# Optimization experiments

Measured on AMD Instinct MI355X. Metric: run time of the kernel, lower is better.

The kernel has to match this reference:

```python
import jax, jax.numpy as jnp
import numpy as np

B, T, C = 4, 1024, 1024
HEAD_SIZE = 64
H = C // HEAD_SIZE
N_LAYER, LAYER_ID = 24, 12
D_MIX_LORA, D_DECAY_LORA = 32, 64
HEAD_SIZE_DIVISOR = 8
LN_EPS = 1e-5 * HEAD_SIZE_DIVISOR ** 2


def setup_inputs() -> dict:
    key = jax.random.key(0)
    ks = jax.random.split(key, 16)
    x = jax.random.normal(ks[0], (B, T, C), jnp.float32)

    r01 = LAYER_ID / (N_LAYER - 1)          # ratio_0_to_1
    r10 = 1.0 - LAYER_ID / N_LAYER          # ratio_1_to_almost0
    ddd = np.arange(C, dtype=np.float64) / C

    time_maa_x = jnp.asarray((1.0 - ddd ** r10).astype(np.float32))
    time_maa_w = jnp.asarray((1.0 - ddd ** r10).astype(np.float32))
    time_maa_k = jnp.asarray((1.0 - ddd ** r10).astype(np.float32))
    time_maa_v = jnp.asarray((1.0 - (ddd ** r10 + 0.3 * r01)).astype(np.float32))
    time_maa_r = jnp.asarray((1.0 - ddd ** (0.5 * r10)).astype(np.float32))
    time_maa_g = jnp.asarray((1.0 - ddd ** (0.5 * r10)).astype(np.float32))

    n = np.arange(C, dtype=np.float64)
    time_decay = jnp.asarray((-6.0 + 5.0 * (n / (C - 1)) ** (0.7 + 1.3 * r01)).astype(np.float32))
    zigzag = ((n + 1) % 3 - 1) * 0.1
    time_faaaa = jnp.asarray((r01 * (1.0 - n / (C - 1)) + zigzag).astype(np.float32)).reshape(H, HEAD_SIZE)

    u = lambda k, shp: jax.random.uniform(k, shp, jnp.float32, -0.01, 0.01)
    time_maa_w1 = u(ks[1], (C, D_MIX_LORA * 5))   # zeros in orig init; small random for a non-trivial test
    time_maa_w2 = u(ks[2], (5, D_MIX_LORA, C))
    time_decay_w1 = u(ks[3], (C, D_DECAY_LORA))
    time_decay_w2 = u(ks[4], (D_DECAY_LORA, C))

    s = 1.0 / np.sqrt(C)
    Wr = jax.random.normal(ks[5], (C, C), jnp.float32) * s   # stored [in, out]
    Wk = jax.random.normal(ks[6], (C, C), jnp.float32) * s
    Wv = jax.random.normal(ks[7], (C, C), jnp.float32) * s
    Wg = jax.random.normal(ks[8], (C, C), jnp.float32) * s
    Wo = jax.random.normal(ks[9], (C, C), jnp.float32) * s
    ln_w = jnp.ones((C,), jnp.float32)
    ln_b = jnp.zeros((C,), jnp.float32)

    return dict(x=x, time_maa_x=time_maa_x, time_maa_w=time_maa_w, time_maa_k=time_maa_k,
                time_maa_v=time_maa_v, time_maa_r=time_maa_r, time_maa_g=time_maa_g,
                time_maa_w1=time_maa_w1, time_maa_w2=time_maa_w2,
                time_decay=time_decay, time_decay_w1=time_decay_w1, time_decay_w2=time_decay_w2,
                time_faaaa=time_faaaa, Wr=Wr, Wk=Wk, Wv=Wv, Wg=Wg, Wo=Wo, ln_w=ln_w, ln_b=ln_b)


def _wkv6(r, k, v, w, u):
    # r,k,v,w: [B,T,H,N]; u: [H,N]. Data-dependent linear recurrence per head.
    def step(S, inp):               # S: [B,H,N,N] (key dim j, value dim i)
        r_t, k_t, v_t, w_t = inp    # each [B,H,N]
        y = jnp.einsum('bhj,bhji->bhi', r_t, S) \
            + jnp.sum(r_t * u * k_t, axis=-1, keepdims=True) * v_t
        decay = jnp.exp(-jnp.exp(w_t))            # CUDA kernel: w_eff = exp(-exp(w))
        S = decay[..., None] * S + k_t[..., None] * v_t[..., None, :]
        return S, y

    to_t = lambda a: jnp.transpose(a, (1, 0, 2, 3))  # [T,B,H,N]
    S0 = jnp.zeros(r.shape[:1] + (r.shape[2], r.shape[3], r.shape[3]), r.dtype)
    _, ys = jax.lax.scan(step, S0, (to_t(r), to_t(k), to_t(v), to_t(w)))
    return jnp.transpose(ys, (1, 0, 2, 3))            # [B,T,H,N]


def reference(x, time_maa_x, time_maa_w, time_maa_k, time_maa_v, time_maa_r, time_maa_g,
              time_maa_w1, time_maa_w2, time_decay, time_decay_w1, time_decay_w2,
              time_faaaa, Wr, Wk, Wv, Wg, Wo, ln_w, ln_b):
    b, t, c = x.shape
    h, n = H, HEAD_SIZE

    # token shift: ZeroPad2d((0,0,1,-1)) shifts time right by one with zero pad
    xx = jnp.concatenate([jnp.zeros_like(x[:, :1]), x[:, :-1]], axis=1) - x
    xxx = x + xx * time_maa_x
    mix = jnp.tanh(xxx @ time_maa_w1).reshape(b, t, 5, D_MIX_LORA)
    m = jnp.einsum('btsd,sdc->sbtc', mix, time_maa_w2)  # [5,B,T,C]
    xw = x + xx * (time_maa_w + m[0])
    xk = x + xx * (time_maa_k + m[1])
    xv = x + xx * (time_maa_v + m[2])
    xr = x + xx * (time_maa_r + m[3])
    xg = x + xx * (time_maa_g + m[4])

    r = xr @ Wr
    k = xk @ Wk
    v = xv @ Wv
    g = jax.nn.silu(xg @ Wg)
    w = time_decay + jnp.tanh(xw @ time_decay_w1) @ time_decay_w2

    y = _wkv6(r.reshape(b, t, h, n), k.reshape(b, t, h, n),
              v.reshape(b, t, h, n), w.reshape(b, t, h, n), time_faaaa)

    # GroupNorm with n_head groups over channel dim, eps = 1e-5 * divisor^2
    mu = y.mean(-1, keepdims=True)
    var = y.var(-1, keepdims=True)
    yn = ((y - mu) / jnp.sqrt(var + LN_EPS)).reshape(b, t, c) * ln_w + ln_b

    return (yn * g) @ Wo
```

## Files before the change

### kernel.cpp

```cpp
#include <hip/hip_runtime.h>

typedef unsigned short u16;
typedef short short8 __attribute__((ext_vector_type(8)));
typedef short short4v __attribute__((ext_vector_type(4)));
typedef float float4v __attribute__((ext_vector_type(4)));
typedef unsigned uint4v __attribute__((ext_vector_type(4)));

__device__ __forceinline__ float bf2f(u16 h) { return __uint_as_float(((unsigned)h) << 16); }
__device__ __forceinline__ u16 f2bf(float f) {
  unsigned u = __float_as_uint(f);
  unsigned r = (u + 0x7fffu + ((u >> 16) & 1u)) >> 16;
  return (u16)r;
}
__device__ __forceinline__ bool is_f32(const void* probe) {
  return ((const u16*)probe)[0] != 0x3F80;
}
__device__ __forceinline__ float ldin(const void* p, long i, bool f32m) {
  return f32m ? ((const float*)p)[i] : bf2f(((const u16*)p)[i]);
}

typedef __attribute__((address_space(1))) const unsigned int as1_u32;
typedef __attribute__((address_space(3))) unsigned int as3_u32;
__device__ __forceinline__ void gl2lds16(const void* g, void* l) {
  __builtin_amdgcn_global_load_lds((as1_u32*)g, (as3_u32*)l, 16, 0, 0);
}

template <int CTRL>
__device__ __forceinline__ float dpp_add(float x) {
  int s = __builtin_amdgcn_update_dpp(0, __float_as_int(x), CTRL, 0xF, 0xF, true);
  return x + __int_as_float(s);
}

__global__ __launch_bounds__(256) void sentinel_fill(u16* o, long n) {
  long i = (long)blockIdx.x * 256 + threadIdx.x;
  if (i < n) o[i] = 0x42C8;
}

struct TDescArr {
  const void* src[13];
  u16* dst[13];
  int rows[13];
  int cols[13];
  int roff[13];
};

__global__ __launch_bounds__(256) void transpose_all(TDescArr d, const void* probe) {
  bool f32m = is_f32(probe);
  int z = blockIdx.z;
  int rows = d.rows[z], cols = d.cols[z], roff = d.roff[z];
  int bc = blockIdx.x * 32, br = blockIdx.y * 32;
  if (bc >= cols || br >= rows) return;
  const void* src = d.src[z];
  u16* dst = d.dst[z];
  __shared__ u16 tile[32][33];
  int tx = threadIdx.x & 31, ty = threadIdx.x >> 5;
#pragma unroll
  for (int i = 0; i < 32; i += 8)
    tile[ty + i][tx] = f2bf(ldin(src, (long)(roff + br + ty + i) * cols + bc + tx, f32m));
  __syncthreads();
#pragma unroll
  for (int i = 0; i < 32; i += 8)
    dst[(long)(bc + ty + i) * rows + br + tx] = tile[tx][ty + i];
}

__global__ __launch_bounds__(256) void token_shift(const void* __restrict__ x,
                                                   const void* __restrict__ maa_x,
                                                   u16* __restrict__ xxx) {
  bool f32m = is_f32(maa_x);
  long idx = (long)blockIdx.x * 256 + threadIdx.x;
  int c = (int)(idx & 1023);
  int tt = (int)((idx >> 10) & 1023);
  float xv = ldin(x, idx, f32m);
  float xp = tt > 0 ? ldin(x, idx - 1024, f32m) : 0.f;
  xxx[idx] = f2bf(xv + (xp - xv) * ldin(maa_x, c, f32m));
}

template <int EPI>
__device__ __forceinline__ void gemm128_core(const u16* __restrict__ A,
                                             const u16* __restrict__ Bt,
                                             void* __restrict__ Cv, int N, int K,
                                             int m0, int n0, u16* As, u16* Bs,
                                             bool f32m) {
  int t = threadIdx.x, lane = t & 63, w = t >> 6;
  int wm = (w >> 1) * 64, wn = (w & 1) * 64;
  int lr = lane & 15, lk = lane >> 4;
  float4v acc[4][4];
#pragma unroll
  for (int i = 0; i < 4; i++)
#pragma unroll
    for (int j = 0; j < 4; j++) acc[i][j] = (float4v){0.f, 0.f, 0.f, 0.f};
  int srow = t >> 3;
  int scol = ((t & 7) ^ (srow & 7)) * 8;
  const u16* Ag = A + (long)(m0 + srow) * K + scol;
  const u16* Bg = Bt + (long)(n0 + srow) * K + scol;
  int so = w * 512;
  for (int k0 = 0; k0 < K; k0 += 64) {
    __syncthreads();
#pragma unroll
    for (int p = 0; p < 4; p++) {
      gl2lds16(Ag + (long)p * 32 * K + k0, As + p * 2048 + so);
      gl2lds16(Bg + (long)p * 32 * K + k0, Bs + p * 2048 + so);
    }
    __syncthreads();
    short8 af[4][2], bfr[4][2];
#pragma unroll
    for (int i = 0; i < 4; i++) {
      int R = wm + i * 16 + lr;
#pragma unroll
      for (int h = 0; h < 2; h++) {
        int j = h * 4 + lk;
        af[i][h] = *(const short8*)(As + R * 64 + (j ^ (R & 7)) * 8);
      }
    }
#pragma unroll
    for (int i = 0; i < 4; i++) {
      int R = wn + i * 16 + lr;
#pragma unroll
      for (int h = 0; h < 2; h++) {
        int j = h * 4 + lk;
        bfr[i][h] = *(const short8*)(Bs + R * 64 + (j ^ (R & 7)) * 8);
      }
    }
#pragma unroll
    for (int mi2 = 0; mi2 < 4; mi2++)
#pragma unroll
      for (int ni2 = 0; ni2 < 4; ni2++) {
        acc[mi2][ni2] = __builtin_amdgcn_mfma_f32_16x16x32_bf16(
            af[mi2][0], bfr[ni2][0], acc[mi2][ni2], 0, 0, 0);
        acc[mi2][ni2] = __builtin_amdgcn_mfma_f32_16x16x32_bf16(
            af[mi2][1], bfr[ni2][1], acc[mi2][ni2], 0, 0, 0);
      }
  }
#pragma unroll
  for (int mi2 = 0; mi2 < 4; mi2++) {
#pragma unroll
    for (int ni2 = 0; ni2 < 4; ni2++) {
      int col = n0 + wn + ni2 * 16 + lr;
#pragma unroll
      for (int rr = 0; rr < 4; rr++) {
        long row = m0 + wm + mi2 * 16 + lk * 4 + rr;
        float val = acc[mi2][ni2][rr];
        if (EPI == 1) val = val / (1.f + __expf(-val));
        if (EPI == 2 && f32m) ((float*)Cv)[row * N + col] = val;
        else ((u16*)Cv)[row * N + col] = f2bf(val);
      }
    }
  }
}

template <int EPI>
__global__ __launch_bounds__(256, 2) void gemm_big(const u16* __restrict__ A,
                                                   const u16* __restrict__ Bt,
                                                   void* __restrict__ Cv, int M, int N,
                                                   int K, const void* probe) {
  __shared__ alignas(16) u16 As[128 * 64];
  __shared__ alignas(16) u16 Bs[128 * 64];
  int sid = blockIdx.y * gridDim.x + blockIdx.x;
  int per8 = (gridDim.x * gridDim.y) >> 3;
  int L = (sid & 7) * per8 + (sid >> 3);
  int mi = L / gridDim.y, ni = L % gridDim.y;
  bool f32m = (EPI == 2) ? is_f32(probe) : false;
  gemm128_core<EPI>(A, Bt, Cv, N, K, mi * 128, ni * 128, As, Bs, f32m);
}

template <int EPI0, int EPI1>
__global__ __launch_bounds__(256, 2) void gemm_big2(
    const u16* __restrict__ A0, const u16* __restrict__ Bt0, u16* __restrict__ C0,
    const u16* __restrict__ A1, const u16* __restrict__ Bt1, u16* __restrict__ C1,
    int M, int N, int K) {
  __shared__ alignas(16) u16 As[128 * 64];
  __shared__ alignas(16) u16 Bs[128 * 64];
  int z = blockIdx.z;
  int sid = blockIdx.y * gridDim.x + blockIdx.x;
  int per8 = (gridDim.x * gridDim.y) >> 3;
  int L = (sid & 7) * per8 + (sid >> 3);
  int mi = L / gridDim.y, ni = L % gridDim.y;
  if (z == 0)
    gemm128_core<EPI0>(A0, Bt0, C0, N, K, mi * 128, ni * 128, As, Bs, false);
  else
    gemm128_core<EPI1>(A1, Bt1, C1, N, K, mi * 128, ni * 128, As, Bs, false);
}

template <int EPI>
__global__ __launch_bounds__(256) void gemm_wave(const u16* __restrict__ A, int lda,
                                                 const u16* __restrict__ Bt,
                                                 u16* __restrict__ C, int ldc,
                                                 float* dA_, float* dB_, int Ntot,
                                                 int K, const void* aux0,
                                                 const void* probe,
                                                 const void* __restrict__ xin) {
  int t = threadIdx.x, lane = t & 63, w = t >> 6;
  int m0 = blockIdx.x * 64 + w * 16;
  int span = Ntot / gridDim.y;
  int col0 = blockIdx.y * span;
  const u16* Bp = Bt + (long)col0 * K;
  int lr = lane & 15, lk = lane >> 4;
  bool f32m = (EPI >= 2) ? is_f32(probe) : false;
  int nt = span >> 4;
  for (int g0 = 0; g0 < nt; g0 += 4) {
    int gc = (nt - g0 < 4) ? (nt - g0) : 4;
    float4v acc[4];
#pragma unroll
    for (int i = 0; i < 4; i++) acc[i] = (float4v){0.f, 0.f, 0.f, 0.f};
    for (int k0 = 0; k0 < K; k0 += 32) {
      short8 a = *(const short8*)(A + (long)(m0 + lr) * lda + k0 + lk * 8);
      for (int gi = 0; gi < gc; gi++) {
        int n0 = (g0 + gi) * 16;
        short8 b = *(const short8*)(Bp + (long)(n0 + lr) * K + k0 + lk * 8);
        acc[gi] = __builtin_amdgcn_mfma_f32_16x16x32_bf16(a, b, acc[gi], 0, 0, 0);
      }
    }
    for (int gi = 0; gi < gc; gi++) {
      int col = col0 + (g0 + gi) * 16 + lr;
      if (EPI == 3) {
        long r0 = m0 + lk * 4;
        float xv4[4];
#pragma unroll
        for (int rr = 0; rr < 4; rr++)
          xv4[rr] = ldin(xin, (r0 + rr) * 1024 + col, f32m);
        float xpv = ((int)(r0 & 1023) > 0) ? ldin(xin, (r0 - 1) * 1024 + col, f32m) : 0.f;
        float mv = ldin(aux0, col, f32m);
#pragma unroll
        for (int rr = 0; rr < 4; rr++) {
          float xv = xv4[rr];
          float xp = (rr == 0) ? xpv : xv4[rr - 1];
          C[(r0 + rr) * 1024 + col] = f2bf(xv + (xp - xv) * (mv + acc[gi][rr]));
        }
      } else {
#pragma unroll
        for (int rr = 0; rr < 4; rr++) {
          long row = m0 + lk * 4 + rr;
          float val = acc[gi][rr];
          if (EPI == 0) {
            C[row * ldc + col] = f2bf(val);
          } else if (EPI == 1) {
            float vv = fminf(fmaxf(val, -15.f), 15.f);
            float e = __expf(2.f * vv);
            C[row * ldc + col] = f2bf((e - 1.f) / (e + 1.f));
          } else if (EPI == 2) {
            float wv = val + ldin(aux0, col, f32m);
            float ew = __expf(wv);
            if (row < 2048) dA_[row * 1024 + col] = ew;
            else dB_[(row - 2048) * 1024 + col] = ew;
          }
        }
      }
    }
  }
}

__global__ __launch_bounds__(256) void gemm_wave3_pair(
    const u16* __restrict__ A0, const u16* __restrict__ Bt0, u16* __restrict__ C0,
    const void* __restrict__ maa0, const u16* __restrict__ A1,
    const u16* __restrict__ Bt1, u16* __restrict__ C1,
    const void* __restrict__ maa1, const void* probe,
    const void* __restrict__ xin) {
  int z = blockIdx.z;
  const u16* A = z ? A1 : A0;
  const u16* Bt = z ? Bt1 : Bt0;
  u16* C = z ? C1 : C0;
  const void* maa = z ? maa1 : maa0;
  bool f32m = is_f32(probe);
  int t = threadIdx.x, lane = t & 63, w = t >> 6;
  int m0 = blockIdx.x * 64 + w * 16;
  int col0 = blockIdx.y * 32;
  const u16* Bp = Bt + (long)col0 * 32;
  int lr = lane & 15, lk = lane >> 4;
  float4v acc[2];
  acc[0] = (float4v){0.f, 0.f, 0.f, 0.f};
  acc[1] = (float4v){0.f, 0.f, 0.f, 0.f};
  short8 a = *(const short8*)(A + (long)(m0 + lr) * 160 + lk * 8);
#pragma unroll
  for (int gi = 0; gi < 2; gi++) {
    short8 b = *(const short8*)(Bp + (long)(gi * 16 + lr) * 32 + lk * 8);
    acc[gi] = __builtin_amdgcn_mfma_f32_16x16x32_bf16(a, b, acc[gi], 0, 0, 0);
  }
#pragma unroll
  for (int gi = 0; gi < 2; gi++) {
    int col = col0 + gi * 16 + lr;
    long r0 = m0 + lk * 4;
    float xv4[4];
#pragma unroll
    for (int rr = 0; rr < 4; rr++)
      xv4[rr] = ldin(xin, (r0 + rr) * 1024 + col, f32m);
    float xpv = ((int)(r0 & 1023) > 0) ? ldin(xin, (r0 - 1) * 1024 + col, f32m) : 0.f;
    float mv = ldin(maa, col, f32m);
#pragma unroll
    for (int rr = 0; rr < 4; rr++) {
      float xv = xv4[rr];
      float xp = (rr == 0) ? xpv : xv4[rr - 1];
      C[(r0 + rr) * 1024 + col] = f2bf(xv + (xp - xv) * (mv + acc[gi][rr]));
    }
  }
}

__global__ __launch_bounds__(256) void gemm_n64_tanh(const u16* __restrict__ A,
                                                     const u16* __restrict__ Bt,
                                                     u16* __restrict__ C) {
  int t = threadIdx.x, lane = t & 63, w = t >> 6;
  int m0 = blockIdx.x * 16;
  int n0 = w * 16;
  int lr = lane & 15, lk = lane >> 4;
  float4v acc = (float4v){0.f, 0.f, 0.f, 0.f};
  const u16* Ap = A + (long)(m0 + lr) * 1024;
  const u16* Bp = Bt + (long)(n0 + lr) * 1024;
  for (int k0 = 0; k0 < 1024; k0 += 32) {
    short8 a = *(const short8*)(Ap + k0 + lk * 8);
    short8 b = *(const short8*)(Bp + k0 + lk * 8);
    acc = __builtin_amdgcn_mfma_f32_16x16x32_bf16(a, b, acc, 0, 0, 0);
  }
#pragma unroll
  for (int rr = 0; rr < 4; rr++) {
    long row = m0 + lk * 4 + rr;
    float vv = fminf(fmaxf(acc[rr], -15.f), 15.f);
    float e = __expf(2.f * vv);
    C[row * 64 + n0 + lr] = f2bf((e - 1.f) / (e + 1.f));
  }
}

__global__ __launch_bounds__(512) void wkv6_chunk(
    const u16* __restrict__ r, const u16* __restrict__ k, const u16* __restrict__ v,
    const float* __restrict__ ewA, const float* __restrict__ ewB,
    const void* __restrict__ u_, const void* probe, u16* __restrict__ y) {
  bool f32m = is_f32(probe);
  int bh = blockIdx.x;
  int b = bh >> 4, h = bh & 15;
  int tid = threadIdx.x, lane = tid & 63, w = tid >> 6;
  int lr = lane & 15, lk = lane >> 4;

  __shared__ alignas(16) float raw[32][68];
  __shared__ alignas(16) float scc[2][32][68];
  __shared__ alignas(16) u16 Rp[32][72];
  __shared__ alignas(16) u16 Kp[32][72];
  __shared__ alignas(16) u16 KdF[64 * 40 + 56];
  __shared__ alignas(16) u16 Vt[64][40];
  __shared__ alignas(16) u16 Pb[32][40];
  __shared__ alignas(16) u16 Sh[64][72];
  __shared__ alignas(16) u16 Sl[64][72];
  __shared__ float diag32[32];

  const long base = ((long)b << 20) + h * 64;
  const float* ewg =
      (b < 2 ? ewA + (long)b * 1048576 : ewB + (long)(b - 2) * 1048576) + h * 64;

  int tt = tid >> 4, kg4 = tid & 15;
  int ck = (w & 3) * 16 + (lane & 15);
  int cq = lane >> 4;
  float u4[4];
#pragma unroll
  for (int i = 0; i < 4; i++) u4[i] = ldin(u_, h * 64 + kg4 * 4 + i, f32m);

  int kw = (w & 3) * 16, vq = w >> 2;
  int skey = kw + lk * 4;
  int yt = w >> 2, yv = w & 3;

  float4v Sst[2];
  Sst[0] = (float4v){0.f, 0.f, 0.f, 0.f};
  Sst[1] = (float4v){0.f, 0.f, 0.f, 0.f};

  {
    long grow = (long)tt << 10;
    float4v ewq = *(const float4v*)(ewg + grow + kg4 * 4);
    short4v rraw = *(const short4v*)(r + base + grow + kg4 * 4);
    short4v kraw = *(const short4v*)(k + base + grow + kg4 * 4);
    short4v vraw = *(const short4v*)(v + base + grow + kg4 * 4);
    *(float4v*)&raw[tt][kg4 * 4] = ewq;
    __syncthreads();
    if (w < 4) {
      float pseg[8];
      float s = 0.f;
#pragma unroll
      for (int j = 0; j < 8; j++) {
        s += raw[cq * 8 + j][ck];
        pseg[j] = s;
      }
      float tot = pseg[7], x = tot;
      float up = __shfl_up(x, 16);
      if (cq >= 1) x += up;
      up = __shfl_up(x, 32);
      if (cq >= 2) x += up;
      float pre = x - tot;
#pragma unroll
      for (int j = 0; j < 8; j++) scc[0][cq * 8 + j][ck] = pre + pseg[j];
    }
    __syncthreads();
    {
      float pd = 0.f;
      short4v rpv, kpv;
#pragma unroll
      for (int i = 0; i < 4; i++) {
        int key = kg4 * 4 + i;
        float rf = bf2f((u16)rraw[i]);
        float kf = bf2f((u16)kraw[i]);
        float si = scc[0][tt][key];
        float sx = tt ? scc[0][tt - 1][key] : 0.f;
        float sE = scc[0][31][key];
        rpv[i] = (short)f2bf(rf * __expf(-sx));
        kpv[i] = (short)f2bf(kf * __expf(si));
        KdF[key * 40 + ((key >> 3) & 7) * 8 + tt] = f2bf(kf * __expf(si - sE));
        pd = fmaf(rf * u4[i], kf, pd);
      }
      *(short4v*)&Rp[tt][kg4 * 4] = rpv;
      *(short4v*)&Kp[tt][kg4 * 4] = kpv;
      pd = dpp_add<0xB1>(pd);
      pd = dpp_add<0x4E>(pd);
      pd = dpp_add<0x104>(pd);
      pd = dpp_add<0x108>(pd);
      if (kg4 == 0) diag32[tt] = pd;
    }
#pragma unroll
    for (int i = 0; i < 4; i++) Vt[kg4 * 4 + i][tt] = (u16)vraw[i];
#pragma unroll
    for (int vt = 0; vt < 2; vt++) {
      short4v z4 = (short4v){0, 0, 0, 0};
      *(short4v*)&Sh[vq * 32 + vt * 16 + lr][skey] = z4;
      *(short4v*)&Sl[vq * 32 + vt * 16 + lr][skey] = z4;
    }
    __syncthreads();
  }

  for (int ci = 0; ci < 32; ++ci) {
    int c0 = ci << 5;
    int c0n = (ci == 31) ? c0 : c0 + 32;
    int pc = ci & 1, pn = pc ^ 1;
    long grow = (long)(c0n + tt) << 10;
    float4v ewq = *(const float4v*)(ewg + grow + kg4 * 4);
    short4v rraw = *(const short4v*)(r + base + grow + kg4 * 4);
    short4v kraw = *(const short4v*)(k + base + grow + kg4 * 4);
    short4v vraw = *(const short4v*)(v + base + grow + kg4 * 4);

    if (w < 4) {
      int pt = w >> 1, pj = w & 1;
      float4v pacc = (float4v){0.f, 0.f, 0.f, 0.f};
      short8 aP0 = *(const short8*)&Rp[pt * 16 + lr][lk * 8];
      short8 aP1 = *(const short8*)&Rp[pt * 16 + lr][lk * 8 + 32];
      short8 bP0 = *(const short8*)&Kp[pj * 16 + lr][lk * 8];
      short8 bP1 = *(const short8*)&Kp[pj * 16 + lr][lk * 8 + 32];
      pacc = __builtin_amdgcn_mfma_f32_16x16x32_bf16(aP0, bP0, pacc, 0, 0, 0);
      pacc = __builtin_amdgcn_mfma_f32_16x16x32_bf16(aP1, bP1, pacc, 0, 0, 0);
      int jcol = pj * 16 + lr;
#pragma unroll
      for (int rr = 0; rr < 4; rr++) {
        int trow = pt * 16 + lk * 4 + rr;
        float val = (jcol < trow) ? pacc[rr] : (jcol == trow ? diag32[trow] : 0.f);
        Pb[trow][jcol] = f2bf(val);
      }
    }
    *(float4v*)&raw[tt][kg4 * 4] = ewq;
    __syncthreads();

    if (w < 4) {
      float pseg[8];
      float s = 0.f;
#pragma unroll
      for (int j = 0; j < 8; j++) {
        s += raw[cq * 8 + j][ck];
        pseg[j] = s;
      }
      float tot = pseg[7], x = tot;
      float up = __shfl_up(x, 16);
      if (cq >= 1) x += up;
      up = __shfl_up(x, 32);
      if (cq >= 2) x += up;
      float pre = x - tot;
#pragma unroll
      for (int j = 0; j < 8; j++) scc[pn][cq * 8 + j][ck] = pre + pseg[j];
    }
    {
      float4v yacc = (float4v){0.f, 0.f, 0.f, 0.f};
      short8 aY = *(const short8*)&Pb[yt * 16 + lr][lk * 8];
      short8 bY = *(const short8*)&Vt[yv * 16 + lr][lk * 8];
      yacc = __builtin_amdgcn_mfma_f32_16x16x32_bf16(aY, bY, yacc, 0, 0, 0);
      short8 aR0 = *(const short8*)&Rp[yt * 16 + lr][lk * 8];
      short8 aR1 = *(const short8*)&Rp[yt * 16 + lr][lk * 8 + 32];
      short8 bH0 = *(const short8*)&Sh[yv * 16 + lr][lk * 8];
      short8 bH1 = *(const short8*)&Sh[yv * 16 + lr][lk * 8 + 32];
      short8 bL0 = *(const short8*)&Sl[yv * 16 + lr][lk * 8];
      short8 bL1 = *(const short8*)&Sl[yv * 16 + lr][lk * 8 + 32];
      yacc = __builtin_amdgcn_mfma_f32_16x16x32_bf16(aR0, bH0, yacc, 0, 0, 0);
      yacc = __builtin_amdgcn_mfma_f32_16x16x32_bf16(aR1, bH1, yacc, 0, 0, 0);
      yacc = __builtin_amdgcn_mfma_f32_16x16x32_bf16(aR0, bL0, yacc, 0, 0, 0);
      yacc = __builtin_amdgcn_mfma_f32_16x16x32_bf16(aR1, bL1, yacc, 0, 0, 0);
#pragma unroll
      for (int rr = 0; rr < 4; rr++) {
        int trow = yt * 16 + lk * 4 + rr;
        y[base + ((long)(c0 + trow) << 10) + yv * 16 + lr] = f2bf(yacc[rr]);
      }
      int kr = kw + lr;
      short8 aS = *(const short8*)&KdF[kr * 40 + ((kr >> 3) & 7) * 8 + lk * 8];
      short8 bS0 = *(const short8*)&Vt[vq * 32 + lr][lk * 8];
      short8 bS1 = *(const short8*)&Vt[vq * 32 + 16 + lr][lk * 8];
      float4v sa0 = (float4v){0.f, 0.f, 0.f, 0.f};
      float4v sa1 = (float4v){0.f, 0.f, 0.f, 0.f};
      sa0 = __builtin_amdgcn_mfma_f32_16x16x32_bf16(aS, bS0, sa0, 0, 0, 0);
      sa1 = __builtin_amdgcn_mfma_f32_16x16x32_bf16(aS, bS1, sa1, 0, 0, 0);
#pragma unroll
      for (int rr = 0; rr < 4; rr++) {
        float cl = __expf(-scc[pc][31][skey + rr]);
        Sst[0][rr] = fmaf(Sst[0][rr], cl, sa0[rr]);
        Sst[1][rr] = fmaf(Sst[1][rr], cl, sa1[rr]);
      }
    }
    __syncthreads();

    {
      float pd = 0.f;
      short4v rpv, kpv;
#pragma unroll
      for (int i = 0; i < 4; i++) {
        int key = kg4 * 4 + i;
        float rf = bf2f((u16)rraw[i]);
        float kf = bf2f((u16)kraw[i]);
        float si = scc[pn][tt][key];
        float sx = tt ? scc[pn][tt - 1][key] : 0.f;
        float sE = scc[pn][31][key];
        rpv[i] = (short)f2bf(rf * __expf(-sx));
        kpv[i] = (short)f2bf(kf * __expf(si));
        KdF[key * 40 + ((key >> 3) & 7) * 8 + tt] = f2bf(kf * __expf(si - sE));
        pd = fmaf(rf * u4[i], kf, pd);
      }
      *(short4v*)&Rp[tt][kg4 * 4] = rpv;
      *(short4v*)&Kp[tt][kg4 * 4] = kpv;
      pd = dpp_add<0xB1>(pd);
      pd = dpp_add<0x4E>(pd);
      pd = dpp_add<0x104>(pd);
      pd = dpp_add<0x108>(pd);
      if (kg4 == 0) diag32[tt] = pd;
    }
#pragma unroll
    for (int i = 0; i < 4; i++) Vt[kg4 * 4 + i][tt] = (u16)vraw[i];
#pragma unroll
    for (int vt = 0; vt < 2; vt++) {
      short4v hi4, lo4;
#pragma unroll
      for (int rr = 0; rr < 4; rr++) {
        u16 hv = f2bf(Sst[vt][rr]);
        hi4[rr] = (short)hv;
        lo4[rr] = (short)f2bf(Sst[vt][rr] - bf2f(hv));
      }
      *(short4v*)&Sh[vq * 32 + vt * 16 + lr][skey] = hi4;
      *(short4v*)&Sl[vq * 32 + vt * 16 + lr][skey] = lo4;
    }
    __syncthreads();
  }
}

__global__ __launch_bounds__(256) void gn_gate(const u16* __restrict__ y,
                                               const u16* __restrict__ g,
                                               const void* __restrict__ lnw,
                                               const void* __restrict__ lnb,
                                               const void* probe,
                                               u16* __restrict__ out) {
  bool f32m = is_f32(probe);
  int gid = blockIdx.x * 4 + (threadIdx.x >> 6);
  int lane = threadIdx.x & 63;
  int h = gid & 15;
  long row = gid >> 4;
  long off = row * 1024 + h * 64 + lane;
  float val = bf2f(y[off]);
  float s = val, sq = val * val;
#pragma unroll
  for (int m = 1; m < 64; m <<= 1) {
    s += __shfl_xor(s, m);
    sq += __shfl_xor(sq, m);
  }
  float mean = s * (1.f / 64.f);
  float var = fmaxf(sq * (1.f / 64.f) - mean * mean, 0.f);
  float inv = rsqrtf(var + 6.4e-4f);
  int c = h * 64 + lane;
  float yn = (val - mean) * inv * ldin(lnw, c, f32m) + ldin(lnb, c, f32m);
  out[off] = f2bf(yn * bf2f(g[off]));
}

extern "C" void kernel_launch(void* const* d_in, const int* in_sizes, int n_in,
                              void* d_out, int out_size, void* d_ws, size_t ws_size,
                              hipStream_t stream) {
  const void* x = d_in[0];
  const void* maaX = d_in[1];
  const void* maa_s[5] = {d_in[2], d_in[3], d_in[4], d_in[5], d_in[6]};
  const void* w1 = d_in[7];
  const void* w2 = d_in[8];
  const void* tdec = d_in[9];
  const void* dw1 = d_in[10];
  const void* dw2 = d_in[11];
  const void* faaaa = d_in[12];
  const void* Wr = d_in[13];
  const void* Wk = d_in[14];
  const void* Wv = d_in[15];
  const void* Wg = d_in[16];
  const void* Wo = d_in[17];
  const void* lnw = d_in[18];
  const void* lnb = d_in[19];

  const long oWoT = 4194304;
  const long ow1T = 5242880;
  const long odw1T = 5406720;
  const long odw2T = 5472256;
  const long ow2T = 5537792;
  const long omixb = 5701632;
  const long owtan = 6356992;
  const long oxxxg = 6619136;
  const long omx = 10813440;
  const long orb = 15007744;
  const long okb = 19202048;
  const long ovb = 23396352;
  const long oyb = 27590656;
  const long oend = 31784960;
  const size_t needed = (size_t)oend * 2;

  if (ws_size < needed) {
    sentinel_fill<<<dim3((unsigned)((out_size + 255) / 256)), 256, 0, stream>>>(
        (u16*)d_out, out_size);
    return;
  }

  u16* W = (u16*)d_ws;
  u16* WrT = W;
  u16* WkT = W + 1048576;
  u16* WvT = W + 2097152;
  u16* WgT = W + 3145728;
  u16* WoT = W + oWoT;
  u16* w1T = W + ow1T;
  u16* dw1T = W + odw1T;
  u16* dw2T = W + odw2T;
  u16* w2T = W + ow2T;
  u16* mixb = W + omixb;
  u16* wtan = W + owtan;
  u16* xxxg = W + oxxxg;
  u16* mx = W + omx;
  u16* rbuf = W + orb;
  u16* kbuf = W + okb;
  u16* vbuf = W + ovb;
  u16* ybuf = W + oyb;
  float* dA_ = (float*)W;
  float* dB_ = (float*)(W + omx);
  u16* gated = mx;

  TDescArr td;
  const void* s5[5] = {Wr, Wk, Wv, Wg, Wo};
  u16* t5[5] = {WrT, WkT, WvT, WgT, WoT};
  for (int i = 0; i < 13; i++) td.roff[i] = 0;
  for (int i = 0; i < 5; i++) {
    td.src[i] = s5[i]; td.dst[i] = t5[i]; td.rows[i] = 1024; td.cols[i] = 1024;
  }
  td.src[5] = w1;  td.dst[5] = w1T;  td.rows[5] = 1024; td.cols[5] = 160;
  td.src[6] = dw1; td.dst[6] = dw1T; td.rows[6] = 1024; td.cols[6] = 64;
  td.src[7] = dw2; td.dst[7] = dw2T; td.rows[7] = 64;   td.cols[7] = 1024;
  for (int s = 0; s < 5; s++) {
    td.src[8 + s] = w2;
    td.dst[8 + s] = w2T + s * 1024 * 32;
    td.rows[8 + s] = 32; td.cols[8 + s] = 1024; td.roff[8 + s] = s * 32;
  }

  transpose_all<<<dim3(32, 32, 13), 256, 0, stream>>>(td, maaX);
  token_shift<<<dim3(16384), 256, 0, stream>>>(x, maaX, xxxg);
  gemm_wave<1><<<dim3(64, 10), 256, 0, stream>>>(xxxg, 1024, w1T, mixb, 160, nullptr,
                                                 nullptr, 160, 1024, nullptr, nullptr,
                                                 nullptr);
  gemm_wave3_pair<<<dim3(64, 32, 2), 256, 0, stream>>>(
      mixb + 3 * 32, w2T + 3 * 32768, mx, maa_s[3],
      mixb + 1 * 32, w2T + 1 * 32768, ybuf, maa_s[1], maaX, x);
  gemm_big2<0, 0><<<dim3(32, 8, 2), 256, 0, stream>>>(mx, WrT, rbuf, ybuf, WkT, kbuf,
                                                      4096, 1024, 1024);
  gemm_wave3_pair<<<dim3(64, 32, 2), 256, 0, stream>>>(
      mixb + 2 * 32, w2T + 2 * 32768, mx, maa_s[2],
      mixb + 4 * 32, w2T + 4 * 32768, ybuf, maa_s[4], maaX, x);
  gemm_big2<0, 1><<<dim3(32, 8, 2), 256, 0, stream>>>(mx, WvT, vbuf, ybuf, WgT, xxxg,
                                                      4096, 1024, 1024);
  gemm_wave<3><<<dim3(64, 32), 256, 0, stream>>>(mixb + 0 * 32, 160, w2T + 0 * 32768,
                                                 mx, 1024, nullptr, nullptr, 1024, 32,
                                                 maa_s[0], maaX, x);
  gemm_n64_tanh<<<dim3(256), 256, 0, stream>>>(mx, dw1T, wtan);
  gemm_wave<2><<<dim3(64, 16), 256, 0, stream>>>(wtan, 64, dw2T, nullptr, 0, dA_, dB_,
                                                 1024, 64, tdec, maaX, nullptr);
  wkv6_chunk<<<dim3(64), 512, 0, stream>>>(rbuf, kbuf, vbuf, dA_, dB_, faaaa, maaX,
                                           ybuf);
  gn_gate<<<dim3(16384), 256, 0, stream>>>(ybuf, xxxg, lnw, lnb, maaX, gated);
  gemm_big<2><<<dim3(32, 8), 256, 0, stream>>>(gated, WoT, d_out, 4096, 1024, 1024, maaX);
}
```

Measured before the change: 353.5 us.

## Split WKV6 scan into parallel segment-state pass and per-segment output pass

The single-pass chunked WKV6 kernel, which ran one block per (batch, head) over 32 sequential chunks, is split in two. The first kernel computes per-segment state contributions and decay products for three of the four 256-token segments. The second kernel runs 256 blocks; each combines the preceding segment states and then processes its own 8 chunks. This adds parallelism, since the original kernel used only 64 blocks on a GPU with many more CUs. The cost is an extra launch, scratch traffic through the output buffer, redundant prefix combination, and splitting the state into bf16 hi/lo parts at each segment start.

```diff
diff --git a/kernel.cpp b/kernel.cpp
--- a/kernel.cpp
+++ b/kernel.cpp
@@ -318,12 +318,112 @@
   }
 }
 
-__global__ __launch_bounds__(512) void wkv6_chunk(
+__global__ __launch_bounds__(512) void wkv6_pass1(
+    const u16* __restrict__ k, const u16* __restrict__ v,
+    const float* __restrict__ ewA, const float* __restrict__ ewB,
+    float* __restrict__ Ascr, float* __restrict__ Dscr) {
+  int bx = blockIdx.x;
+  int g = bx >> 6, bh = bx & 63;
+  int b = bh >> 4, h = bh & 15;
+  int tid = threadIdx.x, lane = tid & 63, w = tid >> 6;
+  int lr = lane & 15, lk = lane >> 4;
+
+  __shared__ alignas(16) float raw[32][68];
+  __shared__ alignas(16) float sck[32][68];
+  __shared__ alignas(16) u16 KdF[64 * 40 + 56];
+  __shared__ alignas(16) u16 Vt[64][40];
+
+  const long base = ((long)b << 20) + h * 64;
+  const float* ewg =
+      (b < 2 ? ewA + (long)b * 1048576 : ewB + (long)(b - 2) * 1048576) + h * 64;
+
+  int tt = tid >> 4, kg4 = tid & 15;
+  int ck = (w & 3) * 16 + (lane & 15), cq = lane >> 4;
+  int kw = (w & 3) * 16, vq = w >> 2;
+  int skey = kw + lk * 4;
+
+  float4v Sst[2];
+  Sst[0] = (float4v){0.f, 0.f, 0.f, 0.f};
+  Sst[1] = (float4v){0.f, 0.f, 0.f, 0.f};
+  float Dacc[4] = {1.f, 1.f, 1.f, 1.f};
+
+  for (int cc = g * 8; cc < g * 8 + 8; ++cc) {
+    long grow = (long)(cc * 32 + tt) << 10;
+    float4v ewq = *(const float4v*)(ewg + grow + kg4 * 4);
+    short4v kraw = *(const short4v*)(k + base + grow + kg4 * 4);
+    short4v vraw = *(const short4v*)(v + base + grow + kg4 * 4);
+    __syncthreads();
+    *(float4v*)&raw[tt][kg4 * 4] = ewq;
+    __syncthreads();
+    if (w < 4) {
+      float pseg[8];
+      float s = 0.f;
+#pragma unroll
+      for (int j = 0; j < 8; j++) {
+        s += raw[cq * 8 + j][ck];
+        pseg[j] = s;
+      }
+      float tot = pseg[7], x = tot;
+      float up = __shfl_up(x, 16);
+      if (cq >= 1) x += up;
+      up = __shfl_up(x, 32);
+      if (cq >= 2) x += up;
+      float pre = x - tot;
+#pragma unroll
+      for (int j = 0; j < 8; j++) sck[cq * 8 + j][ck] = pre + pseg[j];
+    }
+    __syncthreads();
+    {
+#pragma unroll
+      for (int i = 0; i < 4; i++) {
+        int key = kg4 * 4 + i;
+        float kf = bf2f((u16)kraw[i]);
+        float si = sck[tt][key];
+        float sE = sck[31][key];
+        KdF[key * 40 + ((key >> 3) & 7) * 8 + tt] = f2bf(kf * __expf(si - sE));
+        Vt[key][tt] = (u16)vraw[i];
+      }
+    }
+    __syncthreads();
+    {
+      int kr = kw + lr;
+      short8 aS = *(const short8*)&KdF[kr * 40 + ((kr >> 3) & 7) * 8 + lk * 8];
+      short8 bS0 = *(const short8*)&Vt[vq * 32 + lr][lk * 8];
+      short8 bS1 = *(const short8*)&Vt[vq * 32 + 16 + lr][lk * 8];
+      float4v sa0 = (float4v){0.f, 0.f, 0.f, 0.f};
+      float4v sa1 = (float4v){0.f, 0.f, 0.f, 0.f};
+      sa0 = __builtin_amdgcn_mfma_f32_16x16x32_bf16(aS, bS0, sa0, 0, 0, 0);
+      sa1 = __builtin_amdgcn_mfma_f32_16x16x32_bf16(aS, bS1, sa1, 0, 0, 0);
+#pragma unroll
+      for (int rr = 0; rr < 4; rr++) {
+        float cl = __expf(-sck[31][skey + rr]);
+        Sst[0][rr] = fmaf(Sst[0][rr], cl, sa0[rr]);
+        Sst[1][rr] = fmaf(Sst[1][rr], cl, sa1[rr]);
+        Dacc[rr] *= cl;
+      }
+    }
+  }
+  float* Ab = Ascr + ((long)(bh * 3 + g) << 12);
+#pragma unroll
+  for (int vt = 0; vt < 2; vt++)
+#pragma unroll
+    for (int rr = 0; rr < 4; rr++)
+      Ab[(skey + rr) * 64 + vq * 32 + vt * 16 + lr] = Sst[vt][rr];
+  if (vq == 0 && lr == 0) {
+#pragma unroll
+    for (int rr = 0; rr < 4; rr++)
+      Dscr[(bh * 3 + g) * 64 + skey + rr] = Dacc[rr];
+  }
+}
+
+__global__ __launch_bounds__(512) void wkv6_pass3(
     const u16* __restrict__ r, const u16* __restrict__ k, const u16* __restrict__ v,
     const float* __restrict__ ewA, const float* __restrict__ ewB,
-    const void* __restrict__ u_, const void* probe, u16* __restrict__ y) {
+    const void* __restrict__ u_, const void* probe, u16* __restrict__ y,
+    const float* __restrict__ Ascr, const float* __restrict__ Dscr) {
   bool f32m = is_f32(probe);
-  int bh = blockIdx.x;
+  int bx = blockIdx.x;
+  int g = bx >> 6, bh = bx & 63;
   int b = bh >> 4, h = bh & 15;
   int tid = threadIdx.x, lane = tid & 63, w = tid >> 6;
   int lr = lane & 15, lk = lane >> 4;
@@ -357,9 +457,21 @@
   float4v Sst[2];
   Sst[0] = (float4v){0.f, 0.f, 0.f, 0.f};
   Sst[1] = (float4v){0.f, 0.f, 0.f, 0.f};
+  for (int gg = 0; gg < g; ++gg) {
+    const float* Ab = Ascr + ((long)(bh * 3 + gg) << 12);
+    const float* Db = Dscr + (bh * 3 + gg) * 64;
+#pragma unroll
+    for (int rr = 0; rr < 4; rr++) {
+      float d = Db[skey + rr];
+      Sst[0][rr] = fmaf(Sst[0][rr], d, Ab[(skey + rr) * 64 + vq * 32 + lr]);
+      Sst[1][rr] = fmaf(Sst[1][rr], d, Ab[(skey + rr) * 64 + vq * 32 + 16 + lr]);
+    }
+  }
+
+  int cbase = g * 8;
 
   {
-    long grow = (long)tt << 10;
+    long grow = (long)(cbase * 32 + tt) << 10;
     float4v ewq = *(const float4v*)(ewg + grow + kg4 * 4);
     short4v rraw = *(const short4v*)(r + base + grow + kg4 * 4);
     short4v kraw = *(const short4v*)(k + base + grow + kg4 * 4);
@@ -412,16 +524,22 @@
     for (int i = 0; i < 4; i++) Vt[kg4 * 4 + i][tt] = (u16)vraw[i];
 #pragma unroll
     for (int vt = 0; vt < 2; vt++) {
-      short4v z4 = (short4v){0, 0, 0, 0};
-      *(short4v*)&Sh[vq * 32 + vt * 16 + lr][skey] = z4;
-      *(short4v*)&Sl[vq * 32 + vt * 16 + lr][skey] = z4;
-    }
-    __syncthreads();
-  }
-
-  for (int ci = 0; ci < 32; ++ci) {
-    int c0 = ci << 5;
-    int c0n = (ci == 31) ? c0 : c0 + 32;
+      short4v hi4, lo4;
+#pragma unroll
+      for (int rr = 0; rr < 4; rr++) {
+        u16 hv = f2bf(Sst[vt][rr]);
+        hi4[rr] = (short)hv;
+        lo4[rr] = (short)f2bf(Sst[vt][rr] - bf2f(hv));
+      }
+      *(short4v*)&Sh[vq * 32 + vt * 16 + lr][skey] = hi4;
+      *(short4v*)&Sl[vq * 32 + vt * 16 + lr][skey] = lo4;
+    }
+    __syncthreads();
+  }
+
+  for (int ci = 0; ci < 8; ++ci) {
+    int c0 = (cbase + ci) << 5;
+    int c0n = (ci == 7) ? c0 : c0 + 32;
     int pc = ci & 1, pn = pc ^ 1;
     long grow = (long)(c0n + tt) << 10;
     float4v ewq = *(const float4v*)(ewg + grow + kg4 * 4);
@@ -635,6 +753,8 @@
   float* dA_ = (float*)W;
   float* dB_ = (float*)(W + omx);
   u16* gated = mx;
+  float* Ascr = (float*)d_out;
+  float* Dscr = Ascr + 786432;
 
   TDescArr td;
   const void* s5[5] = {Wr, Wk, Wv, Wg, Wo};
@@ -673,8 +793,9 @@
   gemm_n64_tanh<<<dim3(256), 256, 0, stream>>>(mx, dw1T, wtan);
   gemm_wave<2><<<dim3(64, 16), 256, 0, stream>>>(wtan, 64, dw2T, nullptr, 0, dA_, dB_,
                                                  1024, 64, tdec, maaX, nullptr);
-  wkv6_chunk<<<dim3(64), 512, 0, stream>>>(rbuf, kbuf, vbuf, dA_, dB_, faaaa, maaX,
-                                           ybuf);
+  wkv6_pass1<<<dim3(192), 512, 0, stream>>>(kbuf, vbuf, dA_, dB_, Ascr, Dscr);
+  wkv6_pass3<<<dim3(256), 512, 0, stream>>>(rbuf, kbuf, vbuf, dA_, dB_, faaaa, maaX,
+                                            ybuf, Ascr, Dscr);
   gn_gate<<<dim3(16384), 256, 0, stream>>>(ybuf, xxxg, lnw, lnb, maaX, gated);
   gemm_big<2><<<dim3(32, 8), 256, 0, stream>>>(gated, WoT, d_out, 4096, 1024, 1024, maaX);
 }
```

Result: faster. 318.3 us (-9.9%).
